# Kernel tuning notes

Measured on AMD Instinct MI355X. Metric: run time of the kernel, lower is better.

The kernel has to match this reference:

```python
import jax, jax.numpy as jnp
import numpy as np

GRID = 7  # kernel hard-codes 7x7 spatial grid
NEG = -1.0e20


def setup_inputs() -> dict:
    key = jax.random.key(0)
    ks = jax.random.split(key, 6)
    N, Cq, Cv = 512, 64, 512
    B = N * GRID
    return {
        "qH": jax.random.normal(ks[0], (B, GRID, Cq), dtype=jnp.float32),
        "kH": jax.random.normal(ks[1], (B, Cq, GRID), dtype=jnp.float32),
        "vH": jax.random.normal(ks[2], (B, Cv, GRID), dtype=jnp.float32),
        "qW": jax.random.normal(ks[3], (B, GRID, Cq), dtype=jnp.float32),
        "kW": jax.random.normal(ks[4], (B, Cq, GRID), dtype=jnp.float32),
        "vW": jax.random.normal(ks[5], (B, Cv, GRID), dtype=jnp.float32),
        "N": N,
    }


def reference(qH, kH, vH, qW, kW, vW, N):
    # H-direction tensors are folded as batch index bw = n*7 + w; attend over h-axis.
    # W-direction tensors are folded as batch index bh = n*7 + h; attend over w-axis.
    Cq = qH.shape[-1]
    Cv = vH.shape[1]
    qHr = qH.reshape(N, GRID, GRID, Cq)   # [n, w, h, c]
    kHr = kH.reshape(N, GRID, Cq, GRID)   # [n, w, c, j]
    vHr = vH.reshape(N, GRID, Cv, GRID)   # [n, w, c, j]
    qWr = qW.reshape(N, GRID, GRID, Cq)   # [n, h, w, c]
    kWr = kW.reshape(N, GRID, Cq, GRID)   # [n, h, c, y]
    vWr = vW.reshape(N, GRID, Cv, GRID)   # [n, h, c, y]

    # Column (H-axis) logits, with self-position (j == h) masked to -1e20.
    eH = jnp.einsum("nwhc,nwcj->nwhj", qHr, kHr)          # [n, w, h, j]
    eye = jnp.eye(GRID, dtype=bool)[None, None]            # mask on (h, j)
    eH = jnp.where(eye, jnp.float32(NEG), eH)
    # Row (W-axis) logits, no mask.
    eW = jnp.einsum("nhwc,nhcy->nhwy", qWr, kWr)          # [n, h, w, y]

    # Fused softmax over the 14 concatenated H+W logits per (n, h, w).
    logits = jnp.concatenate([eH.transpose(0, 2, 1, 3), eW], axis=-1)  # [n, h, w, 14]
    p = jax.nn.softmax(logits, axis=-1)
    pH = p[..., :GRID].transpose(0, 2, 1, 3)               # [n, w, h, j]
    pW = p[..., GRID:]                                     # [n, h, w, y]

    outH = jnp.einsum("nwhj,nwcj->nchw", pH, vHr)
    outW = jnp.einsum("nhwy,nhcy->nchw", pW, vWr)
    return outH + outW                                     # [n, Cv, 7, 7]
```

## Files before the change

kernel.cpp:

```cpp
#include <hip/hip_runtime.h>


#define NEGINF (-1e20f)

constexpr int QK_SLICE = 7 * 7 * 64;
constexpr int V_SLICE  = 7 * 512 * 7;


__global__ __launch_bounds__(512, 4) void fused_axial(
    const float* __restrict__ qH, const float* __restrict__ kH,
    const float* __restrict__ vH, const float* __restrict__ qW,
    const float* __restrict__ kW, const float* __restrict__ vW,
    float* __restrict__ out)
{
    __shared__ float sm[15288];
    float* U = sm;
    float* P = sm + 14504;

    const int n = blockIdx.x;
    const int t = threadIdx.x;

    float* qHs = U;
    float* kHs = U + 3332;
    float* qWs = U + 6524;
    float* kWs = U + 9856;

    {
        const float* srcQH = qH + n * QK_SLICE;
        const float* srcKH = kH + n * QK_SLICE;
        const float* srcQW = qW + n * QK_SLICE;
        const float* srcKW = kW + n * QK_SLICE;
        for (int it = t; it < 784; it += 512) {
            int wh = it >> 4;
            int c  = (it & 15) << 2;
            float4 v0 = ((const float4*)srcQH)[it];
            *(float4*)(qHs + wh * 68 + c) = v0;
            float4 v1 = ((const float4*)srcQW)[it];
            *(float4*)(qWs + wh * 68 + c) = v1;
            int w = it / 112;
            int r = (it - w * 112) << 2;
            float4 v2 = ((const float4*)srcKH)[it];
            *(float4*)(kHs + w * 456 + r) = v2;
            float4 v3 = ((const float4*)srcKW)[it];
            *(float4*)(kWs + w * 456 + r) = v3;
        }
    }
    __syncthreads();

    for (int d = t; d < 686; d += 512) {
        const bool isH = d < 343;
        int dd = isH ? d : d - 343;
        int a   = dd / 49;
        int rem = dd - a * 49;
        int b   = rem / 7;
        int j   = rem - b * 7;
        const float* qrow  = (isH ? qHs : qWs) + (a * 7 + b) * 68;
        const float* kbase = (isH ? kHs : kWs) + a * 456 + j;
        float e = 0.f;
        #pragma unroll
        for (int c = 0; c < 64; c += 4) {
            float4 qv = *(const float4*)(qrow + c);
            e += qv.x * kbase[c * 7];
            e += qv.y * kbase[c * 7 + 7];
            e += qv.z * kbase[c * 7 + 14];
            e += qv.w * kbase[c * 7 + 21];
        }
        if (isH) {
            if (b == j) e = NEGINF;
            P[(b * 7 + a) * 16 + j] = e;
        } else {
            P[(a * 7 + b) * 16 + 7 + j] = e;
        }
    }
    __syncthreads();

    if (t < 49) {
        float* row = P + t * 16;
        float l[14];
        float m = -3.4e38f;
        #pragma unroll
        for (int k = 0; k < 14; ++k) { l[k] = row[k]; m = fmaxf(m, l[k]); }
        float s = 0.f;
        #pragma unroll
        for (int k = 0; k < 14; ++k) { l[k] = __expf(l[k] - m); s += l[k]; }
        float inv = 1.f / s;
        #pragma unroll
        for (int k = 0; k < 14; ++k) row[k] = l[k] * inv;
    }
    __syncthreads();

    const int g  = t / 49;
    const int hw = t - g * 49;
    const int h  = hw / 7;
    const int w  = hw - h * 7;
    const bool active = (t < 490);

    float pr[14];
    if (active) {
        #pragma unroll
        for (int k = 0; k < 14; ++k) pr[k] = P[hw * 16 + k];
    }

    float* As = U;
    float* Bs = U + 7252;
    float* outn = out + n * V_SLICE;
    const float* vHn = vH + n * V_SLICE;
    const float* vWn = vW + n * V_SLICE;

    for (int chunk = 0; chunk < 4; ++chunk) {
        const int c0 = chunk * 128;
        __syncthreads();
        for (int it = t; it < 3136; it += 512) {
            int arr = it / 1568;
            int rem = it - arr * 1568;
            int i   = rem / 224;
            int q4  = rem - i * 224;
            int r   = q4 << 2;
            const float* src = (arr == 0 ? vHn : vWn) + i * 3584 + c0 * 7 + r;
            float4 val = *(const float4*)src;
            float* dst = (arr == 0 ? As : Bs) + i * 1036;
            const float* vv = (const float*)&val;
            #pragma unroll
            for (int u = 0; u < 4; ++u) {
                int rr = r + u;
                int cl = rr / 7;
                int jj = rr - cl * 7;
                dst[cl * 8 + jj] = vv[u];
            }
        }
        __syncthreads();
        if (active) {
            #pragma unroll
            for (int i = 0; i < 13; ++i) {
                int cl = g + 10 * i;
                if (cl < 128) {
                    const float* arow = As + w * 1036 + cl * 8;
                    const float* brow = Bs + h * 1036 + cl * 8;
                    float4 a0 = *(const float4*)(arow);
                    float4 a1 = *(const float4*)(arow + 4);
                    float4 b0 = *(const float4*)(brow);
                    float4 b1 = *(const float4*)(brow + 4);
                    float acc;
                    acc  = pr[0] * a0.x + pr[1] * a0.y + pr[2] * a0.z + pr[3] * a0.w;
                    acc += pr[4] * a1.x + pr[5] * a1.y + pr[6] * a1.z;
                    acc += pr[7] * b0.x + pr[8] * b0.y + pr[9] * b0.z + pr[10] * b0.w;
                    acc += pr[11] * b1.x + pr[12] * b1.y + pr[13] * b1.z;
                    outn[(c0 + cl) * 49 + hw] = acc;
                }
            }
        }
    }
}

extern "C" void kernel_launch(void* const* d_in, const int* in_sizes, int n_in,
                              void* d_out, int out_size, void* d_ws, size_t ws_size,
                              hipStream_t stream) {
    const float* qH = (const float*)d_in[0];
    const float* kH = (const float*)d_in[1];
    const float* vH = (const float*)d_in[2];
    const float* qW = (const float*)d_in[3];
    const float* kW = (const float*)d_in[4];
    const float* vW = (const float*)d_in[5];
    float* out = (float*)d_out;
    fused_axial<<<512, 512, 0, stream>>>(qH, kH, vH, qW, kW, vW, out);
}
```

Measured before the change: 183.9 us.

## Split each sample across two blocks, prefetch V in registers, shrink shared memory

Each sample now runs in two blocks, each computing half of the output channels, so the grid is 1024 blocks of 512 threads. Shared memory is cut to about 30KB and the launch bound raised to 8 blocks per SM to allow more resident blocks. V is loaded in 64-channel chunks, transposed to channel-contiguous rows, and held in registers so the next chunk's global loads overlap the current chunk's compute. Q is now read straight from global memory during the logits dot product, and the output loop computes four channels per thread with float4 shared loads. The cost is that Q/K loads and the softmax are done twice per sample, and register pressure rises.

```diff
diff --git a/kernel.cpp b/kernel.cpp
--- a/kernel.cpp
+++ b/kernel.cpp
@@ -6,76 +6,105 @@
 constexpr int QK_SLICE = 7 * 7 * 64;
 constexpr int V_SLICE  = 7 * 512 * 7;
 
+#define DECODE(q6v, arr, wj, w, j)        \
+    const int arr = (q6v) >= 49;          \
+    const int wj  = (q6v) - 49 * arr;     \
+    const int w   = (wj * 37) >> 8;       \
+    const int j   = wj - 7 * w;
 
-__global__ __launch_bounds__(512, 4) void fused_axial(
+__global__ __launch_bounds__(512, 8) void fused_axial(
     const float* __restrict__ qH, const float* __restrict__ kH,
     const float* __restrict__ vH, const float* __restrict__ qW,
     const float* __restrict__ kW, const float* __restrict__ vW,
     float* __restrict__ out)
 {
-    __shared__ float sm[15288];
-    float* U = sm;
-    float* P = sm + 14504;
+    __shared__ float sm[7609];
+    float* As = sm;
+    float* Bs = sm + 3388;
+    float* P  = sm + 6776;
 
-    const int n = blockIdx.x;
-    const int t = threadIdx.x;
+    const int bid  = blockIdx.x;
+    const int work = (bid & 7) * 128 + (bid >> 3);
+    const int n    = work >> 1;
+    const int hf   = work & 1;
+    const int t    = threadIdx.x;
 
-    float* qHs = U;
-    float* kHs = U + 3332;
-    float* qWs = U + 6524;
-    float* kWs = U + 9856;
+    const float* qHn = qH + n * QK_SLICE;
+    const float* kHn = kH + n * QK_SLICE;
+    const float* qWn = qW + n * QK_SLICE;
+    const float* kWn = kW + n * QK_SLICE;
+    const float* vHn = vH + n * V_SLICE;
+    const float* vWn = vW + n * V_SLICE;
+    float* outn = out + n * V_SLICE;
+
+    const int c   = t & 63;
+    const int q6b = t >> 6;
 
     {
-        const float* srcQH = qH + n * QK_SLICE;
-        const float* srcKH = kH + n * QK_SLICE;
-        const float* srcQW = qW + n * QK_SLICE;
-        const float* srcKW = kW + n * QK_SLICE;
-        for (int it = t; it < 784; it += 512) {
-            int wh = it >> 4;
-            int c  = (it & 15) << 2;
-            float4 v0 = ((const float4*)srcQH)[it];
-            *(float4*)(qHs + wh * 68 + c) = v0;
-            float4 v1 = ((const float4*)srcQW)[it];
-            *(float4*)(qWs + wh * 68 + c) = v1;
-            int w = it / 112;
-            int r = (it - w * 112) << 2;
-            float4 v2 = ((const float4*)srcKH)[it];
-            *(float4*)(kHs + w * 456 + r) = v2;
-            float4 v3 = ((const float4*)srcKW)[it];
-            *(float4*)(kWs + w * 456 + r) = v3;
+        float r[13];
+        #pragma unroll
+        for (int u = 0; u < 13; ++u) {
+            const int q6 = q6b + 8 * u;
+            if (u < 12 || q6 < 98) {
+                DECODE(q6, arr, wj, w, j)
+                r[u] = *((arr ? kWn : kHn) + w * 448 + c * 7 + j);
+            }
+        }
+        #pragma unroll
+        for (int u = 0; u < 13; ++u) {
+            const int q6 = q6b + 8 * u;
+            if (u < 12 || q6 < 98) {
+                DECODE(q6, arr, wj, w, j)
+                (arr ? Bs : As)[w * 484 + j * 68 + c] = r[u];
+            }
+        }
+    }
+
+    float vr[13];
+    {
+        const int c7 = (hf * 256 + c) * 7;
+        #pragma unroll
+        for (int u = 0; u < 13; ++u) {
+            const int q6 = q6b + 8 * u;
+            if (u < 12 || q6 < 98) {
+                DECODE(q6, arr, wj, w, j)
+                vr[u] = *((arr ? vWn : vHn) + w * 3584 + c7 + j);
+            }
         }
     }
     __syncthreads();
 
-    for (int d = t; d < 686; d += 512) {
-        const bool isH = d < 343;
-        int dd = isH ? d : d - 343;
-        int a   = dd / 49;
-        int rem = dd - a * 49;
-        int b   = rem / 7;
-        int j   = rem - b * 7;
-        const float* qrow  = (isH ? qHs : qWs) + (a * 7 + b) * 68;
-        const float* kbase = (isH ? kHs : kWs) + a * 456 + j;
-        float e = 0.f;
-        #pragma unroll
-        for (int c = 0; c < 64; c += 4) {
-            float4 qv = *(const float4*)(qrow + c);
-            e += qv.x * kbase[c * 7];
-            e += qv.y * kbase[c * 7 + 7];
-            e += qv.z * kbase[c * 7 + 14];
-            e += qv.w * kbase[c * 7 + 21];
-        }
-        if (isH) {
-            if (b == j) e = NEGINF;
-            P[(b * 7 + a) * 16 + j] = e;
-        } else {
-            P[(a * 7 + b) * 16 + 7 + j] = e;
-        }
+    {
+        auto do_dot = [&](int d) {
+            const bool isH = d < 343;
+            const int dd  = isH ? d : d - 343;
+            const int a   = (dd * 1339) >> 16;
+            const int rem = dd - a * 49;
+            const int b   = (rem * 37) >> 8;
+            const int j   = rem - 7 * b;
+            const float* qrow = (isH ? qHn : qWn) + (a * 7 + b) * 64;
+            const float* krow = (isH ? As : Bs) + a * 484 + j * 68;
+            float e = 0.f;
+            #pragma unroll
+            for (int cc = 0; cc < 64; cc += 4) {
+                float4 qv = *(const float4*)(qrow + cc);
+                float4 kv = *(const float4*)(krow + cc);
+                e += qv.x * kv.x + qv.y * kv.y + qv.z * kv.z + qv.w * kv.w;
+            }
+            if (isH) {
+                if (b == j) e = NEGINF;
+                P[(b * 7 + a) * 17 + j] = e;
+            } else {
+                P[(a * 7 + b) * 17 + 7 + j] = e;
+            }
+        };
+        do_dot(t);
+        if (t < 174) do_dot(512 + t);
     }
     __syncthreads();
 
     if (t < 49) {
-        float* row = P + t * 16;
+        float* row = P + t * 17;
         float l[14];
         float m = -3.4e38f;
         #pragma unroll
@@ -89,66 +118,70 @@
     }
     __syncthreads();
 
-    const int g  = t / 49;
+    const int g  = (t * 1339) >> 16;
     const int hw = t - g * 49;
-    const int h  = hw / 7;
-    const int w  = hw - h * 7;
+    const int h  = (hw * 37) >> 8;
+    const int w  = hw - 7 * h;
     const bool active = (t < 490);
 
     float pr[14];
     if (active) {
         #pragma unroll
-        for (int k = 0; k < 14; ++k) pr[k] = P[hw * 16 + k];
+        for (int k = 0; k < 14; ++k) pr[k] = P[hw * 17 + k];
     }
 
-    float* As = U;
-    float* Bs = U + 7252;
-    float* outn = out + n * V_SLICE;
-    const float* vHn = vH + n * V_SLICE;
-    const float* vWn = vW + n * V_SLICE;
-
     for (int chunk = 0; chunk < 4; ++chunk) {
-        const int c0 = chunk * 128;
-        __syncthreads();
-        for (int it = t; it < 3136; it += 512) {
-            int arr = it / 1568;
-            int rem = it - arr * 1568;
-            int i   = rem / 224;
-            int q4  = rem - i * 224;
-            int r   = q4 << 2;
-            const float* src = (arr == 0 ? vHn : vWn) + i * 3584 + c0 * 7 + r;
-            float4 val = *(const float4*)src;
-            float* dst = (arr == 0 ? As : Bs) + i * 1036;
-            const float* vv = (const float*)&val;
+        #pragma unroll
+        for (int u = 0; u < 13; ++u) {
+            const int q6 = q6b + 8 * u;
+            if (u < 12 || q6 < 98) {
+                DECODE(q6, arr, wj, w2, j2)
+                (arr ? Bs : As)[w2 * 484 + j2 * 68 + c] = vr[u];
+            }
+        }
+        if (chunk < 3) {
+            const int c7n = (hf * 256 + (chunk + 1) * 64 + c) * 7;
             #pragma unroll
-            for (int u = 0; u < 4; ++u) {
-                int rr = r + u;
-                int cl = rr / 7;
-                int jj = rr - cl * 7;
-                dst[cl * 8 + jj] = vv[u];
+            for (int u = 0; u < 13; ++u) {
+                const int q6 = q6b + 8 * u;
+                if (u < 12 || q6 < 98) {
+                    DECODE(q6, arr, wj, w2, j2)
+                    vr[u] = *((arr ? vWn : vHn) + w2 * 3584 + c7n + j2);
+                }
             }
         }
         __syncthreads();
+
         if (active) {
+            const int c0 = hf * 256 + chunk * 64;
+            const float* arow = As + w * 484;
+            const float* brow = Bs + h * 484;
             #pragma unroll
-            for (int i = 0; i < 13; ++i) {
-                int cl = g + 10 * i;
-                if (cl < 128) {
-                    const float* arow = As + w * 1036 + cl * 8;
-                    const float* brow = Bs + h * 1036 + cl * 8;
-                    float4 a0 = *(const float4*)(arow);
-                    float4 a1 = *(const float4*)(arow + 4);
-                    float4 b0 = *(const float4*)(brow);
-                    float4 b1 = *(const float4*)(brow + 4);
-                    float acc;
-                    acc  = pr[0] * a0.x + pr[1] * a0.y + pr[2] * a0.z + pr[3] * a0.w;
-                    acc += pr[4] * a1.x + pr[5] * a1.y + pr[6] * a1.z;
-                    acc += pr[7] * b0.x + pr[8] * b0.y + pr[9] * b0.z + pr[10] * b0.w;
-                    acc += pr[11] * b1.x + pr[12] * b1.y + pr[13] * b1.z;
-                    outn[(c0 + cl) * 49 + hw] = acc;
+            for (int it = 0; it < 2; ++it) {
+                if (it == 0 || g < 6) {
+                    const int cl4 = (g + 10 * it) * 4;
+                    float4 acc = make_float4(0.f, 0.f, 0.f, 0.f);
+                    #pragma unroll
+                    for (int j2 = 0; j2 < 7; ++j2) {
+                        float4 av = *(const float4*)(arow + j2 * 68 + cl4);
+                        acc.x += pr[j2] * av.x; acc.y += pr[j2] * av.y;
+                        acc.z += pr[j2] * av.z; acc.w += pr[j2] * av.w;
+                    }
+                    #pragma unroll
+                    for (int j2 = 0; j2 < 7; ++j2) {
+                        float4 bv = *(const float4*)(brow + j2 * 68 + cl4);
+                        acc.x += pr[7 + j2] * bv.x; acc.y += pr[7 + j2] * bv.y;
+                        acc.z += pr[7 + j2] * bv.z; acc.w += pr[7 + j2] * bv.w;
+                    }
+                    float* o = outn + (c0 + cl4) * 49 + hw;
+                    o[0]   = acc.x;
+                    o[49]  = acc.y;
+                    o[98]  = acc.z;
+                    o[147] = acc.w;
                 }
             }
         }
+        if (chunk < 3) __syncthreads();
     }
 }
 
@@ -162,5 +195,5 @@
     const float* kW = (const float*)d_in[4];
     const float* vW = (const float*)d_in[5];
     float* out = (float*)d_out;
-    fused_axial<<<512, 512, 0, stream>>>(qH, kH, vH, qW, kW, vW, out);
+    fused_axial<<<1024, 512, 0, stream>>>(qH, kH, vH, qW, kW, vW, out);
 }
```

Result: slower. 248.3 us (+35.0%).
